# Kernel optimization log

Measured on AMD Instinct MI355X. Metric: run time of the kernel, lower is better.

Reference implementation:

```python
import math
import jax, jax.numpy as jnp
import numpy as np

N_HEADS = 16

def setup_inputs() -> dict:
    key = jax.random.key(0)
    qkv = jax.random.normal(key, (4, 3072, 2048), dtype=jnp.float32)
    return {"qkv": qkv}

def reference(qkv):
    bs, width, length = qkv.shape
    ch = width // (3 * N_HEADS)
    # [bs*H, 3*ch, L] -> split into q, k, v of [bs*H, ch, L]
    qkv_r = qkv.reshape(bs * N_HEADS, 3 * ch, length)
    q, k, v = qkv_r[:, :ch], qkv_r[:, ch:2 * ch], qkv_r[:, 2 * ch:]
    scale = 1.0 / math.sqrt(math.sqrt(ch))
    # scores: [bs*H, T, S]
    weight = jnp.einsum('bct,bcs->bts', q * scale, k * scale)
    weight = jax.nn.softmax(weight, axis=-1)
    a = jnp.einsum('bts,bcs->bct', weight, v)
    return a.reshape(bs, -1, length)
```

## Files before the change

### kernel.cpp

```cpp
#include <hip/hip_runtime.h>
#include <cstdint>

typedef _Float16 half8 __attribute__((ext_vector_type(8)));
typedef _Float16 half4v __attribute__((ext_vector_type(4)));
typedef float f32x4 __attribute__((ext_vector_type(4)));

#define HSTRIDE 131072
#define KOFF    (64 * HSTRIDE)
#define VOFF    (2 * (size_t)64 * HSTRIDE)

__device__ __forceinline__ float fast_exp2(float x) {
#if __has_builtin(__builtin_amdgcn_exp2f)
    return __builtin_amdgcn_exp2f(x);
#else
    return exp2f(x);
#endif
}

__device__ __forceinline__ void load_lds16(const _Float16* g, _Float16* l) {
    auto* g1 = reinterpret_cast<const __attribute__((address_space(1))) uint32_t*>(
        reinterpret_cast<uintptr_t>(g));
    auto* l3 = reinterpret_cast<__attribute__((address_space(3))) uint32_t*>(
        reinterpret_cast<uintptr_t>(l));
    __builtin_amdgcn_global_load_lds(g1, l3, 16, 0, 0);
}

__global__ __launch_bounds__(256) void prep_kernel(const float* __restrict__ qkv,
                                                   _Float16* __restrict__ ws)
{
    __shared__ _Float16 L[64 * 136];

    const int tid   = threadIdx.x;
    const int bid   = blockIdx.x;
    const int type  = bid >> 10;
    const int hc    = bid & 1023;
    const int head  = hc >> 4;
    const int chunk = hc & 15;
    const int b4    = head >> 4;
    const int h     = head & 15;

    const float* src = qkv + (((size_t)(b4 * 3072 + h * 192 + type * 64)) << 11) + chunk * 128;

#pragma unroll
    for (int k = 0; k < 8; ++k) {
        int idx = k * 256 + tid;
        int c   = idx >> 5;
        int t4  = (idx & 31) << 2;
        float4 f = *(const float4*)&src[((size_t)c << 11) + t4];
        half4v hv;
        hv[0] = (_Float16)f.x; hv[1] = (_Float16)f.y;
        hv[2] = (_Float16)f.z; hv[3] = (_Float16)f.w;
        *(half4v*)&L[c * 136 + t4] = hv;
    }
    __syncthreads();

    if (type < 2) {
#pragma unroll
        for (int k = 0; k < 4; ++k) {
            int idx = k * 256 + tid;
            int t = idx >> 3, g = idx & 7;
            half8 v;
#pragma unroll
            for (int u = 0; u < 8; ++u) v[u] = L[(g * 8 + u) * 136 + t];
            size_t o;
            if (type == 0) {
                o = (size_t)head * HSTRIDE + (size_t)(chunk * 128 + t) * 64 + g * 8;
            } else {
                int s = chunk * 128 + t;
                o = KOFF + (size_t)head * HSTRIDE + (size_t)s * 64 + ((g ^ (s & 7)) << 3);
            }
            *(half8*)&ws[o] = v;
        }
    } else {
#pragma unroll
        for (int k = 0; k < 4; ++k) {
            int idx = k * 256 + tid;
            int c = idx >> 4, gs = idx & 15;
            half8 v = *(const half8*)&L[c * 136 + gs * 8];
            size_t o = VOFF + (size_t)head * HSTRIDE + (size_t)chunk * 8192
                     + (size_t)c * 128 + ((gs ^ (c & 15)) << 3);
            *(half8*)&ws[o] = v;
        }
    }
}

__launch_bounds__(256, 2)
__global__ void attn_kernel(const _Float16* __restrict__ ws, float* __restrict__ out)
{
    __shared__ __align__(16) _Float16 sK[128 * 64];
    __shared__ __align__(16) _Float16 sV[64 * 128];
    __shared__ __align__(16) _Float16 sP[128 * 128];

    const int tid  = threadIdx.x;
    const int lane = tid & 63;
    const int wave = tid >> 6;
    const int l15  = lane & 15;
    const int quad = lane >> 4;

    const int bid  = blockIdx.x;
    const int head = bid & 63;
    const int tblk = bid >> 6;
    const int T0   = tblk * 128;
    const int b4   = head >> 4;
    const int h    = head & 15;

    const _Float16* Qt = ws + (size_t)head * HSTRIDE;
    const _Float16* Kt = ws + KOFF + (size_t)head * HSTRIDE;
    const _Float16* Vt = ws + VOFF + (size_t)head * HSTRIDE;

    half8 qf[2][2];
#pragma unroll
    for (int mt = 0; mt < 2; ++mt)
#pragma unroll
        for (int ks = 0; ks < 2; ++ks)
            qf[mt][ks] = *(const half8*)&Qt[(size_t)(T0 + wave * 32 + mt * 16 + l15) * 64
                                            + ks * 32 + quad * 8];

    const float kScale = 0.125f * 1.44269504088896340736f;

    f32x4 Oacc[2][4];
#pragma unroll
    for (int mt = 0; mt < 2; ++mt)
#pragma unroll
        for (int ct = 0; ct < 4; ++ct) Oacc[mt][ct] = (f32x4)0.f;
    float lacc[2][4];
#pragma unroll
    for (int mt = 0; mt < 2; ++mt)
#pragma unroll
        for (int r = 0; r < 4; ++r) lacc[mt][r] = 0.f;

    for (int it = 0; it < 16; ++it) {
        const int s0 = it << 7;
        __syncthreads();

        const _Float16* kg = Kt + ((size_t)s0 << 6);
        const _Float16* vg = Vt + ((size_t)s0 << 6);
#pragma unroll
        for (int i = 0; i < 4; ++i) {
            int off = i * 2048 + wave * 512;
            load_lds16(kg + off + lane * 8, &sK[off]);
            load_lds16(vg + off + lane * 8, &sV[off]);
        }
        __syncthreads();

        f32x4 Sc[2][8];
#pragma unroll
        for (int mt = 0; mt < 2; ++mt)
#pragma unroll
            for (int nt = 0; nt < 8; ++nt) Sc[mt][nt] = (f32x4)0.f;
#pragma unroll
        for (int nt = 0; nt < 8; ++nt) {
            const int srow = nt * 16 + l15;
#pragma unroll
            for (int ks = 0; ks < 2; ++ks) {
                half8 kb = *(const half8*)&sK[srow * 64 + (((ks * 4 + quad) ^ (srow & 7)) << 3)];
                Sc[0][nt] = __builtin_amdgcn_mfma_f32_16x16x32_f16(qf[0][ks], kb, Sc[0][nt], 0, 0, 0);
                Sc[1][nt] = __builtin_amdgcn_mfma_f32_16x16x32_f16(qf[1][ks], kb, Sc[1][nt], 0, 0, 0);
            }
        }

#pragma unroll
        for (int mt = 0; mt < 2; ++mt) {
            const int trow_base = wave * 32 + mt * 16 + 4 * quad;
#pragma unroll
            for (int nt = 0; nt < 8; ++nt) {
                const int g = 2 * nt + (l15 >> 3);
#pragma unroll
                for (int r = 0; r < 4; ++r) {
                    float p = fast_exp2(Sc[mt][nt][r] * kScale);
                    lacc[mt][r] += p;
                    const int trow = trow_base + r;
                    sP[trow * 128 + (((g ^ (trow & 15)) << 3) | (l15 & 7))] = (_Float16)p;
                }
            }
        }

        half8 pa[2][4];
#pragma unroll
        for (int mt = 0; mt < 2; ++mt) {
            const int trow = wave * 32 + mt * 16 + l15;
#pragma unroll
            for (int ks = 0; ks < 4; ++ks)
                pa[mt][ks] = *(const half8*)&sP[trow * 128 + (((ks * 4 + quad) ^ l15) << 3)];
        }
#pragma unroll
        for (int ct = 0; ct < 4; ++ct) {
            const int c = ct * 16 + l15;
#pragma unroll
            for (int ks = 0; ks < 4; ++ks) {
                half8 vb = *(const half8*)&sV[c * 128 + (((ks * 4 + quad) ^ l15) << 3)];
                Oacc[0][ct] = __builtin_amdgcn_mfma_f32_16x16x32_f16(pa[0][ks], vb, Oacc[0][ct], 0, 0, 0);
                Oacc[1][ct] = __builtin_amdgcn_mfma_f32_16x16x32_f16(pa[1][ks], vb, Oacc[1][ct], 0, 0, 0);
            }
        }
    }

    float inv[2][4];
#pragma unroll
    for (int mt = 0; mt < 2; ++mt)
#pragma unroll
        for (int r = 0; r < 4; ++r) {
            float v = lacc[mt][r];
#pragma unroll
            for (int mask = 1; mask <= 8; mask <<= 1) v += __shfl_xor(v, mask, 64);
            inv[mt][r] = 1.f / v;
        }

    float* ob = out + (((size_t)(b4 * 1024 + h * 64)) << 11) + T0 + wave * 32;
#pragma unroll
    for (int mt = 0; mt < 2; ++mt)
#pragma unroll
        for (int ct = 0; ct < 4; ++ct) {
            f32x4 o = Oacc[mt][ct];
#pragma unroll
            for (int r = 0; r < 4; ++r) o[r] *= inv[mt][r];
            *(f32x4*)&ob[((size_t)(ct * 16 + l15) << 11) + mt * 16 + 4 * quad] = o;
        }
}

extern "C" void kernel_launch(void* const* d_in, const int* in_sizes, int n_in,
                              void* d_out, int out_size, void* d_ws, size_t ws_size,
                              hipStream_t stream) {
    const float* qkv = (const float*)d_in[0];
    float* out = (float*)d_out;
    _Float16* ws = (_Float16*)d_ws;
    prep_kernel<<<dim3(3072), dim3(256), 0, stream>>>(qkv, ws);
    attn_kernel<<<dim3(1024), dim3(256), 0, stream>>>(ws, out);
}
```

Measured before the change: 266.6 us.

## Transpose QK MFMA, fold softmax scale into Q prep, pack P writes

The score MFMA now takes K as the A operand and Q as the B operand, so each lane holds four consecutive key columns of one query row. This allows packed 64-bit fp16 stores of P via cvt_pkrtz and row sums kept as a single per-lane scalar. The softmax scale and log2e factor are applied to Q in the prep kernel, which removes a multiply per score. Prep keeps fp32 data in LDS and converts with packed RTZ. V skips LDS entirely. LDS offsets are precomputed outside the loop. Row sums are reduced through a small LDS array instead of xor shuffles. RTZ rounding replaces round-to-nearest, which changes numerics slightly.

```diff
diff --git a/kernel.cpp b/kernel.cpp
--- a/kernel.cpp
+++ b/kernel.cpp
@@ -2,19 +2,20 @@
 #include <cstdint>
 
 typedef _Float16 half8 __attribute__((ext_vector_type(8)));
-typedef _Float16 half4v __attribute__((ext_vector_type(4)));
+typedef __fp16 fp16x2 __attribute__((ext_vector_type(2)));
 typedef float f32x4 __attribute__((ext_vector_type(4)));
 
 #define HSTRIDE 131072
-#define KOFF    (64 * HSTRIDE)
-#define VOFF    (2 * (size_t)64 * HSTRIDE)
+#define KOFF    ((size_t)64 * HSTRIDE)
+#define VOFF    ((size_t)128 * HSTRIDE)
 
 __device__ __forceinline__ float fast_exp2(float x) {
-#if __has_builtin(__builtin_amdgcn_exp2f)
     return __builtin_amdgcn_exp2f(x);
-#else
-    return exp2f(x);
-#endif
+}
+
+__device__ __forceinline__ uint32_t pkrtz(float a, float b) {
+    fp16x2 h = __builtin_amdgcn_cvt_pkrtz(a, b);
+    return __builtin_bit_cast(uint32_t, h);
 }
 
 __device__ __forceinline__ void load_lds16(const _Float16* g, _Float16* l) {
@@ -28,58 +29,68 @@
 __global__ __launch_bounds__(256) void prep_kernel(const float* __restrict__ qkv,
                                                    _Float16* __restrict__ ws)
 {
-    __shared__ _Float16 L[64 * 136];
-
-    const int tid   = threadIdx.x;
-    const int bid   = blockIdx.x;
-    const int type  = bid >> 10;
-    const int hc    = bid & 1023;
-    const int head  = hc >> 4;
-    const int chunk = hc & 15;
-    const int b4    = head >> 4;
-    const int h     = head & 15;
-
-    const float* src = qkv + (((size_t)(b4 * 3072 + h * 192 + type * 64)) << 11) + chunk * 128;
-
-#pragma unroll
-    for (int k = 0; k < 8; ++k) {
-        int idx = k * 256 + tid;
-        int c   = idx >> 5;
-        int t4  = (idx & 31) << 2;
-        float4 f = *(const float4*)&src[((size_t)c << 11) + t4];
-        half4v hv;
-        hv[0] = (_Float16)f.x; hv[1] = (_Float16)f.y;
-        hv[2] = (_Float16)f.z; hv[3] = (_Float16)f.w;
-        *(half4v*)&L[c * 136 + t4] = hv;
-    }
-    __syncthreads();
-
-    if (type < 2) {
+    __shared__ float Lf[64 * 132];
+
+    const int tid = threadIdx.x;
+    const int bid = blockIdx.x;
+    const float kQ = 0.125f * 1.44269504088896340736f;
+
+    if (bid < 2048) {
+        const int type  = bid >> 10;
+        const int head  = (bid >> 4) & 63;
+        const int chunk = bid & 15;
+        const int b4 = head >> 4, h = head & 15;
+        const float* src = qkv + (((size_t)(b4 * 3072 + h * 192 + type * 64)) << 11)
+                         + chunk * 128;
+
+#pragma unroll
+        for (int k = 0; k < 8; ++k) {
+            int idx = k * 256 + tid;
+            int c = idx >> 5;
+            int t4 = (idx & 31) << 2;
+            *(float4*)&Lf[c * 132 + t4] = *(const float4*)&src[((size_t)c << 11) + t4];
+        }
+        __syncthreads();
+
+        const int tl = tid >> 1;
+        const int gh = (tid & 1) * 4;
+        const float scale = (type == 0) ? kQ : 1.0f;
+        const int row = chunk * 128 + tl;
+        const size_t rowbase = ((type == 0) ? (size_t)head * HSTRIDE
+                                            : KOFF + (size_t)head * HSTRIDE)
+                             + (size_t)row * 64;
+#pragma unroll
+        for (int gg = 0; gg < 4; ++gg) {
+            const int g = gh + gg;
+            uint32_t d[4];
+#pragma unroll
+            for (int j = 0; j < 4; ++j) {
+                float a = Lf[(8 * g + 2 * j) * 132 + tl];
+                float b = Lf[(8 * g + 2 * j + 1) * 132 + tl];
+                d[j] = pkrtz(a * scale, b * scale);
+            }
+            const int pos = (type == 0) ? g : (g ^ (tl & 7));
+            *(uint4*)&ws[rowbase + ((size_t)pos << 3)] = make_uint4(d[0], d[1], d[2], d[3]);
+        }
+    } else {
+        const int vb = bid - 2048;
+        const int head = vb >> 4, chunk = vb & 15;
+        const int b4 = head >> 4, h = head & 15;
+        const float* src = qkv + (((size_t)(b4 * 3072 + h * 192 + 128)) << 11) + chunk * 128;
 #pragma unroll
         for (int k = 0; k < 4; ++k) {
-            int idx = k * 256 + tid;
-            int t = idx >> 3, g = idx & 7;
-            half8 v;
-#pragma unroll
-            for (int u = 0; u < 8; ++u) v[u] = L[(g * 8 + u) * 136 + t];
-            size_t o;
-            if (type == 0) {
-                o = (size_t)head * HSTRIDE + (size_t)(chunk * 128 + t) * 64 + g * 8;
-            } else {
-                int s = chunk * 128 + t;
-                o = KOFF + (size_t)head * HSTRIDE + (size_t)s * 64 + ((g ^ (s & 7)) << 3);
-            }
-            *(half8*)&ws[o] = v;
-        }
-    } else {
-#pragma unroll
-        for (int k = 0; k < 4; ++k) {
-            int idx = k * 256 + tid;
-            int c = idx >> 4, gs = idx & 15;
-            half8 v = *(const half8*)&L[c * 136 + gs * 8];
+            const int c  = k * 16 + (tid >> 4);
+            const int gs = tid & 15;
+            const float* p = &src[((size_t)c << 11) + gs * 8];
+            float4 f0 = *(const float4*)&p[0];
+            float4 f1 = *(const float4*)&p[4];
+            uint32_t d0 = pkrtz(f0.x, f0.y);
+            uint32_t d1 = pkrtz(f0.z, f0.w);
+            uint32_t d2 = pkrtz(f1.x, f1.y);
+            uint32_t d3 = pkrtz(f1.z, f1.w);
             size_t o = VOFF + (size_t)head * HSTRIDE + (size_t)chunk * 8192
-                     + (size_t)c * 128 + ((gs ^ (c & 15)) << 3);
-            *(half8*)&ws[o] = v;
+                     + ((size_t)c << 7) + (size_t)((gs ^ (c & 15)) << 3);
+            *(uint4*)&ws[o] = make_uint4(d0, d1, d2, d3);
         }
     }
 }
@@ -90,6 +101,7 @@
     __shared__ __align__(16) _Float16 sK[128 * 64];
     __shared__ __align__(16) _Float16 sV[64 * 128];
     __shared__ __align__(16) _Float16 sP[128 * 128];
+    __shared__ float sL[4][32];
 
     const int tid  = threadIdx.x;
     const int lane = tid & 63;
@@ -108,113 +120,118 @@
     const _Float16* Kt = ws + KOFF + (size_t)head * HSTRIDE;
     const _Float16* Vt = ws + VOFF + (size_t)head * HSTRIDE;
 
-    half8 qf[2][2];
-#pragma unroll
-    for (int mt = 0; mt < 2; ++mt)
+    half8 qb[2][2];
+#pragma unroll
+    for (int nt = 0; nt < 2; ++nt)
 #pragma unroll
         for (int ks = 0; ks < 2; ++ks)
-            qf[mt][ks] = *(const half8*)&Qt[(size_t)(T0 + wave * 32 + mt * 16 + l15) * 64
+            qb[nt][ks] = *(const half8*)&Qt[(size_t)(T0 + wave * 32 + nt * 16 + l15) * 64
                                             + ks * 32 + quad * 8];
 
-    const float kScale = 0.125f * 1.44269504088896340736f;
+    int kb[2];
+#pragma unroll
+    for (int ks = 0; ks < 2; ++ks)
+        kb[ks] = l15 * 64 + (((ks * 4 + quad) ^ (l15 & 7)) << 3);
+    int vbs[4], pb[4];
+#pragma unroll
+    for (int ks = 0; ks < 4; ++ks) {
+        vbs[ks] = l15 * 128 + (((ks * 4 + quad) ^ l15) << 3);
+        pb[ks]  = (wave * 32 + l15) * 128 + (((ks * 4 + quad) ^ l15) << 3);
+    }
+    int pw[8];
+#pragma unroll
+    for (int mt = 0; mt < 8; ++mt)
+        pw[mt] = (wave * 32 + l15) * 128
+               + ((((2 * mt + (quad >> 1)) ^ l15) << 3) + ((quad & 1) << 2));
 
     f32x4 Oacc[2][4];
 #pragma unroll
-    for (int mt = 0; mt < 2; ++mt)
-#pragma unroll
-        for (int ct = 0; ct < 4; ++ct) Oacc[mt][ct] = (f32x4)0.f;
-    float lacc[2][4];
-#pragma unroll
-    for (int mt = 0; mt < 2; ++mt)
-#pragma unroll
-        for (int r = 0; r < 4; ++r) lacc[mt][r] = 0.f;
+    for (int nt = 0; nt < 2; ++nt)
+#pragma unroll
+        for (int ct = 0; ct < 4; ++ct) Oacc[nt][ct] = (f32x4)0.f;
+    float lacc[2] = {0.f, 0.f};
+    const f32x4 fz = (f32x4)0.f;
 
     for (int it = 0; it < 16; ++it) {
-        const int s0 = it << 7;
         __syncthreads();
-
-        const _Float16* kg = Kt + ((size_t)s0 << 6);
-        const _Float16* vg = Vt + ((size_t)s0 << 6);
+        const _Float16* kg = Kt + (size_t)it * 8192;
+        const _Float16* vg = Vt + (size_t)it * 8192;
 #pragma unroll
         for (int i = 0; i < 4; ++i) {
-            int off = i * 2048 + wave * 512;
+            int off = (i * 4 + wave) * 512;
             load_lds16(kg + off + lane * 8, &sK[off]);
             load_lds16(vg + off + lane * 8, &sV[off]);
         }
         __syncthreads();
 
-        f32x4 Sc[2][8];
-#pragma unroll
-        for (int mt = 0; mt < 2; ++mt)
-#pragma unroll
-            for (int nt = 0; nt < 8; ++nt) Sc[mt][nt] = (f32x4)0.f;
-#pragma unroll
-        for (int nt = 0; nt < 8; ++nt) {
-            const int srow = nt * 16 + l15;
-#pragma unroll
-            for (int ks = 0; ks < 2; ++ks) {
-                half8 kb = *(const half8*)&sK[srow * 64 + (((ks * 4 + quad) ^ (srow & 7)) << 3)];
-                Sc[0][nt] = __builtin_amdgcn_mfma_f32_16x16x32_f16(qf[0][ks], kb, Sc[0][nt], 0, 0, 0);
-                Sc[1][nt] = __builtin_amdgcn_mfma_f32_16x16x32_f16(qf[1][ks], kb, Sc[1][nt], 0, 0, 0);
-            }
-        }
-
-#pragma unroll
-        for (int mt = 0; mt < 2; ++mt) {
-            const int trow_base = wave * 32 + mt * 16 + 4 * quad;
-#pragma unroll
-            for (int nt = 0; nt < 8; ++nt) {
-                const int g = 2 * nt + (l15 >> 3);
-#pragma unroll
-                for (int r = 0; r < 4; ++r) {
-                    float p = fast_exp2(Sc[mt][nt][r] * kScale);
-                    lacc[mt][r] += p;
-                    const int trow = trow_base + r;
-                    sP[trow * 128 + (((g ^ (trow & 15)) << 3) | (l15 & 7))] = (_Float16)p;
-                }
-            }
-        }
+        f32x4 Sc[8][2];
+#pragma unroll
+        for (int mt = 0; mt < 8; ++mt) {
+            half8 ka0 = *(const half8*)&sK[kb[0] + mt * 1024];
+            half8 ka1 = *(const half8*)&sK[kb[1] + mt * 1024];
+#pragma unroll
+            for (int nt = 0; nt < 2; ++nt) {
+                f32x4 c0 = __builtin_amdgcn_mfma_f32_16x16x32_f16(ka0, qb[nt][0], fz, 0, 0, 0);
+                Sc[mt][nt] = __builtin_amdgcn_mfma_f32_16x16x32_f16(ka1, qb[nt][1], c0, 0, 0, 0);
+            }
+        }
+
+#pragma unroll
+        for (int mt = 0; mt < 8; ++mt)
+#pragma unroll
+            for (int nt = 0; nt < 2; ++nt) {
+                f32x4 s = Sc[mt][nt];
+                float p0 = fast_exp2(s[0]);
+                float p1 = fast_exp2(s[1]);
+                float p2 = fast_exp2(s[2]);
+                float p3 = fast_exp2(s[3]);
+                lacc[nt] += p0; lacc[nt] += p1; lacc[nt] += p2; lacc[nt] += p3;
+                uint32_t w0 = pkrtz(p0, p1);
+                uint32_t w1 = pkrtz(p2, p3);
+                *(uint2*)&sP[pw[mt] + nt * 2048] = make_uint2(w0, w1);
+            }
 
         half8 pa[2][4];
 #pragma unroll
-        for (int mt = 0; mt < 2; ++mt) {
-            const int trow = wave * 32 + mt * 16 + l15;
+        for (int nt = 0; nt < 2; ++nt)
 #pragma unroll
             for (int ks = 0; ks < 4; ++ks)
-                pa[mt][ks] = *(const half8*)&sP[trow * 128 + (((ks * 4 + quad) ^ l15) << 3)];
-        }
+                pa[nt][ks] = *(const half8*)&sP[pb[ks] + nt * 2048];
 #pragma unroll
         for (int ct = 0; ct < 4; ++ct) {
-            const int c = ct * 16 + l15;
 #pragma unroll
             for (int ks = 0; ks < 4; ++ks) {
-                half8 vb = *(const half8*)&sV[c * 128 + (((ks * 4 + quad) ^ l15) << 3)];
-                Oacc[0][ct] = __builtin_amdgcn_mfma_f32_16x16x32_f16(pa[0][ks], vb, Oacc[0][ct], 0, 0, 0);
-                Oacc[1][ct] = __builtin_amdgcn_mfma_f32_16x16x32_f16(pa[1][ks], vb, Oacc[1][ct], 0, 0, 0);
-            }
-        }
-    }
-
+                half8 vbf = *(const half8*)&sV[vbs[ks] + ct * 2048];
+                Oacc[0][ct] = __builtin_amdgcn_mfma_f32_16x16x32_f16(pa[0][ks], vbf, Oacc[0][ct], 0, 0, 0);
+                Oacc[1][ct] = __builtin_amdgcn_mfma_f32_16x16x32_f16(pa[1][ks], vbf, Oacc[1][ct], 0, 0, 0);
+            }
+        }
+    }
+
+#pragma unroll
+    for (int nt = 0; nt < 2; ++nt) {
+        float v = lacc[nt];
+        v += __shfl_xor(v, 16, 64);
+        v += __shfl_xor(v, 32, 64);
+        if (quad == 0) sL[wave][nt * 16 + l15] = v;
+    }
+    __builtin_amdgcn_s_waitcnt(0);
     float inv[2][4];
 #pragma unroll
-    for (int mt = 0; mt < 2; ++mt)
-#pragma unroll
-        for (int r = 0; r < 4; ++r) {
-            float v = lacc[mt][r];
-#pragma unroll
-            for (int mask = 1; mask <= 8; mask <<= 1) v += __shfl_xor(v, mask, 64);
-            inv[mt][r] = 1.f / v;
-        }
+    for (int nt = 0; nt < 2; ++nt)
+#pragma unroll
+        for (int r = 0; r < 4; ++r)
+            inv[nt][r] = 1.f / sL[wave][nt * 16 + quad * 4 + r];
 
     float* ob = out + (((size_t)(b4 * 1024 + h * 64)) << 11) + T0 + wave * 32;
 #pragma unroll
-    for (int mt = 0; mt < 2; ++mt)
+    for (int nt = 0; nt < 2; ++nt)
 #pragma unroll
         for (int ct = 0; ct < 4; ++ct) {
-            f32x4 o = Oacc[mt][ct];
-#pragma unroll
-            for (int r = 0; r < 4; ++r) o[r] *= inv[mt][r];
-            *(f32x4*)&ob[((size_t)(ct * 16 + l15) << 11) + mt * 16 + 4 * quad] = o;
+            f32x4 o = Oacc[nt][ct];
+#pragma unroll
+            for (int r = 0; r < 4; ++r) o[r] *= inv[nt][r];
+            *(f32x4*)&ob[((size_t)(ct * 16 + l15) << 11) + nt * 16 + quad * 4] = o;
         }
 }
 
```

After: 252.0 us. 1.06x faster.
